# Kernel tuning notes

Measured on AMD Instinct MI355X. Metric: run time of the kernel, lower is better.

## Reference

```python
import jax, jax.numpy as jnp
import numpy as np

N_HEAD = 12

def setup_inputs() -> dict:
    key = jax.random.key(0)
    k1, k2, k3 = jax.random.split(key, 3)
    B, T, C = 4, 2048, 768
    x = jax.random.normal(k1, (B, T, C), dtype=jnp.float32)
    # c_attn params (Linear(n_embd, 3*n_embd)); stored as [in, out] for x @ W
    W_attn = jax.random.normal(k2, (C, 3 * C), dtype=jnp.float32) * (1.0 / np.sqrt(C))
    b_attn = jax.random.normal(k3, (3 * C,), dtype=jnp.float32) * 0.02
    return {"x": x, "W_attn": W_attn, "b_attn": b_attn}

def reference(x, W_attn, b_attn):
    B, T, C = x.shape
    H = N_HEAD
    Dh = C // H
    qkv = x @ W_attn + b_attn                      # [B,T,3C]
    q, k, v = jnp.split(qkv, 3, axis=-1)
    q = q.reshape(B, T, H, Dh)
    k = k.reshape(B, T, H, Dh)
    v = v.reshape(B, T, H, Dh)
    scale = 1.0 / np.sqrt(Dh)
    # scaled QK^T per head: [B,H,T,T]
    scores = jnp.einsum('bqhd,bkhd->bhqk', q * scale, k)
    causal = jnp.tril(jnp.ones((T, T), dtype=bool))  # [T,T]
    # masked-to--inf then ReLU == zero out non-causal and clamp at 0
    p = jnp.where(causal, jnp.maximum(scores, 0.0), 0.0)
    y = jnp.einsum('bhqk,bkhd->bqhd', p, v).reshape(B, T, C)
    return y
```

## Files before the change

kernel.cpp:

```cpp
#include <hip/hip_runtime.h>
#include <cstdint>
#include <cstddef>

typedef unsigned short u16;
typedef unsigned int u32;
typedef __bf16 bf16x8 __attribute__((ext_vector_type(8)));
typedef float f32x4 __attribute__((ext_vector_type(4)));

__device__ __forceinline__ u16 f2bf(float f) {
    unsigned int x = __builtin_bit_cast(unsigned int, f);
    x += 0x7FFFu + ((x >> 16) & 1u);
    return (u16)(x >> 16);
}

__device__ __forceinline__ bf16x8 ldfrag(const u16* p) {
    bf16x8 r;
    __builtin_memcpy(&r, (const u16*)__builtin_assume_aligned(p, 16), 16);
    return r;
}

__device__ __forceinline__ int4 ldg16(const u16* p) {
    int4 r;
    __builtin_memcpy(&r, (const u16*)__builtin_assume_aligned(p, 16), 16);
    return r;
}

__device__ __forceinline__ void async16(u16* lds, const u16* g) {
    __builtin_amdgcn_global_load_lds(
        (const __attribute__((address_space(1))) void*)g,
        (__attribute__((address_space(3))) void*)lds,
        16, 0, 0);
}

__global__ __launch_bounds__(256) void cvt_bf16(const float* __restrict__ in,
                                                u16* __restrict__ out, int n) {
    int i = (blockIdx.x * 256 + threadIdx.x) * 4;
    if (i >= n) return;
    float4 v = *reinterpret_cast<const float4*>(in + i);
    union { u16 e[4]; unsigned long long u; } w;
    w.e[0] = f2bf(v.x); w.e[1] = f2bf(v.y); w.e[2] = f2bf(v.z); w.e[3] = f2bf(v.w);
    *reinterpret_cast<unsigned long long*>(out + i) = w.u;
}

__global__ __launch_bounds__(256) void wt_transpose(const float* __restrict__ W,
                                                    u16* __restrict__ Wt) {
    const int R = 768, Ccols = 2304;
    __shared__ float tile[32][33];
    const int bx = blockIdx.x * 32;
    const int by = blockIdx.y * 32;
    const int tx = threadIdx.x & 31, ty = threadIdx.x >> 5;
    #pragma unroll
    for (int i = 0; i < 32; i += 8)
        tile[ty + i][tx] = W[(size_t)(by + ty + i) * Ccols + bx + tx];
    __syncthreads();
    #pragma unroll
    for (int i = 0; i < 32; i += 8)
        Wt[(size_t)(bx + ty + i) * R + by + tx] = f2bf(tile[tx][ty + i]);
}

__global__ __launch_bounds__(256) void qkv_gemm(const u16* __restrict__ A,
                                                const u16* __restrict__ Bt,
                                                const float* __restrict__ bias,
                                                u16* __restrict__ C) {
    const int N = 2304, K = 768;
    __shared__ __align__(16) u16 sA[128 * 64];
    __shared__ __align__(16) u16 sB[128 * 64];
    const int t = threadIdx.x;
    const int wave = t >> 6, lane = t & 63;
    const int quad = lane >> 4, l16 = lane & 15;
    const int wr = wave >> 1, wc = wave & 1;

    const int bid = blockIdx.x;
    const int xcd = bid & 7;
    const int idx = bid >> 3;
    const int m0 = (xcd * 8 + idx / 18) * 128;
    const int n0 = (idx % 18) * 128;

    const int srow_base = wave * 8 + (lane >> 3);
    const int schunk = lane & 7;
    const int swz = (lane >> 3) & 7;

    f32x4 acc[4][4] = {};

    for (int k0 = 0; k0 < K; k0 += 64) {
        __syncthreads();
        #pragma unroll
        for (int j = 0; j < 4; ++j) {
            const int row = j * 32 + srow_base;
            const int dch = schunk ^ swz;
            async16(sA + j * 2048 + wave * 512, A + (size_t)(m0 + row) * K + k0 + dch * 8);
            async16(sB + j * 2048 + wave * 512, Bt + (size_t)(n0 + row) * K + k0 + dch * 8);
        }
        __syncthreads();

        bf16x8 af[4][2], bfr[4][2];
        const int rsw = l16 & 7;
        #pragma unroll
        for (int i = 0; i < 4; ++i)
            #pragma unroll
            for (int h = 0; h < 2; ++h) {
                af[i][h] = ldfrag(sA + (wr * 64 + i * 16 + l16) * 64 + (((h * 4 + quad) ^ rsw) << 3));
                bfr[i][h] = ldfrag(sB + (wc * 64 + i * 16 + l16) * 64 + (((h * 4 + quad) ^ rsw) << 3));
            }
        #pragma unroll
        for (int h = 0; h < 2; ++h)
            #pragma unroll
            for (int i = 0; i < 4; ++i)
                #pragma unroll
                for (int j = 0; j < 4; ++j)
                    acc[i][j] = __builtin_amdgcn_mfma_f32_16x16x32_bf16(af[i][h], bfr[j][h], acc[i][j], 0, 0, 0);
    }

    #pragma unroll
    for (int i = 0; i < 4; ++i)
        #pragma unroll
        for (int j = 0; j < 4; ++j) {
            const int col = n0 + wc * 64 + j * 16 + l16;
            const float bc = bias[col];
            const float scale = (col < 768) ? 0.125f : 1.0f;
            #pragma unroll
            for (int r = 0; r < 4; ++r) {
                const int row = m0 + wr * 64 + i * 16 + quad * 4 + r;
                C[(size_t)row * N + col] = f2bf((acc[i][j][r] + bc) * scale);
            }
        }
}

__global__ __launch_bounds__(256, 3) void attn_kernel(const u16* __restrict__ qkv,
                                                      float* __restrict__ out) {
    const int T = 2048, C3 = 2304, Cc = 768, Dh = 64;

    const int bid = blockIdx.x;
    const int xcd = bid & 7;
    const int idx = bid >> 3;
    const int hb = xcd * 6 + (idx % 6);
    const int qa = idx / 6;
    const int qb = 31 - qa;
    const int h = hb % 12, b = hb / 12;

    const int t = threadIdx.x;
    const int wave = t >> 6, lane = t & 63;
    const int quad = lane >> 4, l16 = lane & 15;

    __shared__ __align__(16) u32 sVt[2][64 * 36];
    __shared__ __align__(16) u16 sP[128 * 72];

    const u16* qbase = qkv + (size_t)b * T * C3 + (size_t)h * Dh;
    const u16* kbase = qbase + Cc;
    const u16* vbase = qbase + 2 * Cc;

    bf16x8 qf[8][2];
    #pragma unroll
    for (int cg = 0; cg < 8; ++cg) {
        const int qrow = ((cg < 4) ? qa * 64 : (qb * 64 - 64)) + cg * 16 + l16;
        const u16* p = qbase + (size_t)qrow * C3 + quad * 8;
        qf[cg][0] = ldfrag(p);
        qf[cg][1] = ldfrag(p + 32);
    }

    f32x4 oacc[2][4] = {};

    const int tp = t & 31, dg = t >> 5;

    auto loadV = [&](int it, int4& r0, int4& r1) {
        const u16* vp = vbase + (size_t)(it * 64 + 2 * tp) * C3 + dg * 8;
        r0 = ldg16(vp);
        r1 = ldg16(vp + C3);
    };
    auto ldgK = [&](int it, bf16x8& f0, bf16x8& f1) {
        const u16* kp = kbase + (size_t)(it * 64 + wave * 16 + l16) * C3 + quad * 8;
        f0 = ldfrag(kp);
        f1 = ldfrag(kp + 32);
    };
    auto writeV = [&](int bi, const int4& r0, const int4& r1) {
        union { int4 v; u16 e[8]; } ua, ub;
        ua.v = r0; ub.v = r1;
        #pragma unroll
        for (int i = 0; i < 8; ++i)
            sVt[bi][(dg * 8 + i) * 36 + tp] = (u32)ua.e[i] | ((u32)ub.e[i] << 16);
    };

    bf16x8 kc0, kc1, kn0, kn1;
    int4 vc0, vc1, vn0, vn1;

    {
        int4 a0, a1;
        loadV(0, a0, a1);
        ldgK(0, kc0, kc1);
        writeV(0, a0, a1);
    }
    loadV(1, vc0, vc1);
    vn0 = vc0; vn1 = vc1;
    __syncthreads();

    int buf = 0;
    for (int it = 0; it <= qb; ++it) {
        const bool more  = (it < qb);
        const bool more2 = (it + 1 < qb);
        if (more2) loadV(it + 2, vn0, vn1);
        if (more)  ldgK(it + 1, kn0, kn1);

        const bool act_a = (it <= qa);

        const int cg_lo = act_a ? 0 : 4;
        __builtin_amdgcn_s_setprio(1);
        #pragma unroll
        for (int cg = 7; cg >= 0; --cg) {
            if (cg < cg_lo) break;
            f32x4 s = {};
            s = __builtin_amdgcn_mfma_f32_16x16x32_bf16(kc0, qf[cg][0], s, 0, 0, 0);
            s = __builtin_amdgcn_mfma_f32_16x16x32_bf16(kc1, qf[cg][1], s, 0, 0, 0);
            const bool diag = (cg < 4) ? (it == qa) : (it == qb);
            u32 bits[4];
            #pragma unroll
            for (int r = 0; r < 4; ++r) {
                float v = fmaxf(s[r], 0.0f);
                if (diag && (wave * 16 + quad * 4 + r > (cg & 3) * 16 + l16)) v = 0.0f;
                bits[r] = __builtin_bit_cast(u32, v);
            }
            u32 pk[2];
            pk[0] = (bits[1] & 0xFFFF0000u) | (bits[0] >> 16);
            pk[1] = (bits[3] & 0xFFFF0000u) | (bits[2] >> 16);
            __builtin_memcpy((u16*)__builtin_assume_aligned(
                                 sP + (cg * 16 + l16) * 72 + wave * 16 + quad * 4, 8),
                             pk, 8);
        }
        __builtin_amdgcn_s_setprio(0);

        asm volatile("s_waitcnt lgkmcnt(0)" ::: "memory");
        __builtin_amdgcn_s_barrier();
        asm volatile("" ::: "memory");

        const u16* sVb = (const u16*)sVt[buf];
        __builtin_amdgcn_s_setprio(1);
        #pragma unroll
        for (int kk = 0; kk < 2; ++kk) {
            bf16x8 ap1 = ldfrag(sP + (64 + wave * 16 + l16) * 72 + kk * 32 + quad * 8);
            bf16x8 ap0;
            if (act_a) ap0 = ldfrag(sP + (wave * 16 + l16) * 72 + kk * 32 + quad * 8);
            #pragma unroll
            for (int dt = 0; dt < 4; ++dt) {
                bf16x8 bv = ldfrag(sVb + (dt * 16 + l16) * 72 + kk * 32 + quad * 8);
                oacc[1][dt] = __builtin_amdgcn_mfma_f32_16x16x32_bf16(ap1, bv, oacc[1][dt], 0, 0, 0);
                if (act_a)
                    oacc[0][dt] = __builtin_amdgcn_mfma_f32_16x16x32_bf16(ap0, bv, oacc[0][dt], 0, 0, 0);
            }
        }
        __builtin_amdgcn_s_setprio(0);

        if (more) writeV(buf ^ 1, vc0, vc1);

        asm volatile("s_waitcnt lgkmcnt(0)" ::: "memory");
        __builtin_amdgcn_s_barrier();
        asm volatile("" ::: "memory");

        kc0 = kn0; kc1 = kn1;
        vc0 = vn0; vc1 = vn1;
        buf ^= 1;
    }

    #pragma unroll
    for (int g = 0; g < 2; ++g)
        #pragma unroll
        for (int dt = 0; dt < 4; ++dt)
            #pragma unroll
            for (int r = 0; r < 4; ++r) {
                const int tok = (g == 0 ? qa * 64 : qb * 64) + wave * 16 + quad * 4 + r;
                const int c = h * Dh + dt * 16 + l16;
                out[((size_t)b * T + tok) * Cc + c] = oacc[g][dt][r];
            }
}

extern "C" void kernel_launch(void* const* d_in, const int* in_sizes, int n_in,
                              void* d_out, int out_size, void* d_ws, size_t ws_size,
                              hipStream_t stream) {
    const float* x    = (const float*)d_in[0];
    const float* W    = (const float*)d_in[1];
    const float* bias = (const float*)d_in[2];
    float* out = (float*)d_out;

    char* ws = (char*)d_ws;
    const size_t xb_bytes = (size_t)8192 * 768 * 2;
    const size_t wt_bytes = (size_t)2304 * 768 * 2;
    u16* xb  = (u16*)ws;
    u16* Wt  = (u16*)(ws + xb_bytes);
    u16* qkv = (u16*)(ws + xb_bytes + wt_bytes);

    cvt_bf16<<<6144, 256, 0, stream>>>(x, xb, 8192 * 768);
    wt_transpose<<<dim3(72, 24), 256, 0, stream>>>(W, Wt);
    qkv_gemm<<<1152, 256, 0, stream>>>(xb, Wt, bias, qkv);
    attn_kernel<<<768, 256, 0, stream>>>(qkv, out);
}
```

Before: 179.2 us.

## Split paired query blocks into single-block attention CTAs and prefetch GEMM tiles

The attention kernel no longer pairs a short and a long query block per workgroup. It launches one workgroup per 64-row query block, twice as many, ordered longest-first, with half the P shared buffer and fewer registers, and raises the occupancy hint to 5. Separately, the QKV GEMM issues the next k-tile's async loads right after fragments are read into registers, so global loads overlap the MFMAs. The trade-off is that the K/V streams are loaded twice for the split blocks, and load balance now depends on the hardware scheduler instead of the explicit pairing.

```diff
diff --git a/kernel.cpp b/kernel.cpp
--- a/kernel.cpp
+++ b/kernel.cpp
@@ -79,19 +79,24 @@
     const int srow_base = wave * 8 + (lane >> 3);
     const int schunk = lane & 7;
     const int swz = (lane >> 3) & 7;
-
-    f32x4 acc[4][4] = {};
-
-    for (int k0 = 0; k0 < K; k0 += 64) {
-        __syncthreads();
+    const int dch = schunk ^ swz;
+
+    auto stage = [&](int k0) {
         #pragma unroll
         for (int j = 0; j < 4; ++j) {
             const int row = j * 32 + srow_base;
-            const int dch = schunk ^ swz;
             async16(sA + j * 2048 + wave * 512, A + (size_t)(m0 + row) * K + k0 + dch * 8);
             async16(sB + j * 2048 + wave * 512, Bt + (size_t)(n0 + row) * K + k0 + dch * 8);
         }
-        __syncthreads();
+    };
+
+    f32x4 acc[4][4] = {};
+
+    stage(0);
+    for (int k0 = 0; k0 < K; k0 += 64) {
+        asm volatile("s_waitcnt vmcnt(0)" ::: "memory");
+        __builtin_amdgcn_s_barrier();
+        asm volatile("" ::: "memory");
 
         bf16x8 af[4][2], bfr[4][2];
         const int rsw = l16 & 7;
@@ -102,6 +107,13 @@
                 af[i][h] = ldfrag(sA + (wr * 64 + i * 16 + l16) * 64 + (((h * 4 + quad) ^ rsw) << 3));
                 bfr[i][h] = ldfrag(sB + (wc * 64 + i * 16 + l16) * 64 + (((h * 4 + quad) ^ rsw) << 3));
             }
+
+        asm volatile("s_waitcnt lgkmcnt(0)" ::: "memory");
+        __builtin_amdgcn_s_barrier();
+        asm volatile("" ::: "memory");
+
+        if (k0 + 64 < K) stage(k0 + 64);
+
         #pragma unroll
         for (int h = 0; h < 2; ++h)
             #pragma unroll
@@ -126,16 +138,16 @@
         }
 }
 
-__global__ __launch_bounds__(256, 3) void attn_kernel(const u16* __restrict__ qkv,
+__global__ __launch_bounds__(256, 5) void attn_kernel(const u16* __restrict__ qkv,
                                                       float* __restrict__ out) {
     const int T = 2048, C3 = 2304, Cc = 768, Dh = 64;
 
     const int bid = blockIdx.x;
     const int xcd = bid & 7;
     const int idx = bid >> 3;
-    const int hb = xcd * 6 + (idx % 6);
-    const int qa = idx / 6;
-    const int qb = 31 - qa;
+    const int q = 31 - idx / 6;
+    const int gl = idx % 6;
+    const int hb = xcd * 6 + gl;
     const int h = hb % 12, b = hb / 12;
 
     const int t = threadIdx.x;
@@ -143,22 +155,21 @@
     const int quad = lane >> 4, l16 = lane & 15;
 
     __shared__ __align__(16) u32 sVt[2][64 * 36];
-    __shared__ __align__(16) u16 sP[128 * 72];
+    __shared__ __align__(16) u16 sP[64 * 72];
 
     const u16* qbase = qkv + (size_t)b * T * C3 + (size_t)h * Dh;
     const u16* kbase = qbase + Cc;
     const u16* vbase = qbase + 2 * Cc;
 
-    bf16x8 qf[8][2];
-    #pragma unroll
-    for (int cg = 0; cg < 8; ++cg) {
-        const int qrow = ((cg < 4) ? qa * 64 : (qb * 64 - 64)) + cg * 16 + l16;
-        const u16* p = qbase + (size_t)qrow * C3 + quad * 8;
+    bf16x8 qf[4][2];
+    #pragma unroll
+    for (int cg = 0; cg < 4; ++cg) {
+        const u16* p = qbase + (size_t)(q * 64 + cg * 16 + l16) * C3 + quad * 8;
         qf[cg][0] = ldfrag(p);
         qf[cg][1] = ldfrag(p + 32);
     }
 
-    f32x4 oacc[2][4] = {};
+    f32x4 oacc[4] = {};
 
     const int tp = t & 31, dg = t >> 5;
 
@@ -194,28 +205,24 @@
     __syncthreads();
 
     int buf = 0;
-    for (int it = 0; it <= qb; ++it) {
-        const bool more  = (it < qb);
-        const bool more2 = (it + 1 < qb);
+    for (int it = 0; it <= q; ++it) {
+        const bool more  = (it < q);
+        const bool more2 = (it + 1 < q);
         if (more2) loadV(it + 2, vn0, vn1);
         if (more)  ldgK(it + 1, kn0, kn1);
 
-        const bool act_a = (it <= qa);
-
-        const int cg_lo = act_a ? 0 : 4;
+        const bool diag = (it == q);
         __builtin_amdgcn_s_setprio(1);
         #pragma unroll
-        for (int cg = 7; cg >= 0; --cg) {
-            if (cg < cg_lo) break;
+        for (int cg = 0; cg < 4; ++cg) {
             f32x4 s = {};
             s = __builtin_amdgcn_mfma_f32_16x16x32_bf16(kc0, qf[cg][0], s, 0, 0, 0);
             s = __builtin_amdgcn_mfma_f32_16x16x32_bf16(kc1, qf[cg][1], s, 0, 0, 0);
-            const bool diag = (cg < 4) ? (it == qa) : (it == qb);
             u32 bits[4];
             #pragma unroll
             for (int r = 0; r < 4; ++r) {
                 float v = fmaxf(s[r], 0.0f);
-                if (diag && (wave * 16 + quad * 4 + r > (cg & 3) * 16 + l16)) v = 0.0f;
+                if (diag && (wave * 16 + quad * 4 + r > cg * 16 + l16)) v = 0.0f;
                 bits[r] = __builtin_bit_cast(u32, v);
             }
             u32 pk[2];
@@ -235,15 +242,11 @@
         __builtin_amdgcn_s_setprio(1);
         #pragma unroll
         for (int kk = 0; kk < 2; ++kk) {
-            bf16x8 ap1 = ldfrag(sP + (64 + wave * 16 + l16) * 72 + kk * 32 + quad * 8);
-            bf16x8 ap0;
-            if (act_a) ap0 = ldfrag(sP + (wave * 16 + l16) * 72 + kk * 32 + quad * 8);
+            bf16x8 ap = ldfrag(sP + (wave * 16 + l16) * 72 + kk * 32 + quad * 8);
             #pragma unroll
             for (int dt = 0; dt < 4; ++dt) {
                 bf16x8 bv = ldfrag(sVb + (dt * 16 + l16) * 72 + kk * 32 + quad * 8);
-                oacc[1][dt] = __builtin_amdgcn_mfma_f32_16x16x32_bf16(ap1, bv, oacc[1][dt], 0, 0, 0);
-                if (act_a)
-                    oacc[0][dt] = __builtin_amdgcn_mfma_f32_16x16x32_bf16(ap0, bv, oacc[0][dt], 0, 0, 0);
+                oacc[dt] = __builtin_amdgcn_mfma_f32_16x16x32_bf16(ap, bv, oacc[dt], 0, 0, 0);
             }
         }
         __builtin_amdgcn_s_setprio(0);
@@ -260,15 +263,13 @@
     }
 
     #pragma unroll
-    for (int g = 0; g < 2; ++g)
-        #pragma unroll
-        for (int dt = 0; dt < 4; ++dt)
-            #pragma unroll
-            for (int r = 0; r < 4; ++r) {
-                const int tok = (g == 0 ? qa * 64 : qb * 64) + wave * 16 + quad * 4 + r;
-                const int c = h * Dh + dt * 16 + l16;
-                out[((size_t)b * T + tok) * Cc + c] = oacc[g][dt][r];
-            }
+    for (int dt = 0; dt < 4; ++dt)
+        #pragma unroll
+        for (int r = 0; r < 4; ++r) {
+            const int tok = q * 64 + wave * 16 + quad * 4 + r;
+            const int c = h * Dh + dt * 16 + l16;
+            out[((size_t)b * T + tok) * Cc + c] = oacc[dt][r];
+        }
 }
 
 extern "C" void kernel_launch(void* const* d_in, const int* in_sizes, int n_in,
@@ -289,5 +290,5 @@
     cvt_bf16<<<6144, 256, 0, stream>>>(x, xb, 8192 * 768);
     wt_transpose<<<dim3(72, 24), 256, 0, stream>>>(W, Wt);
     qkv_gemm<<<1152, 256, 0, stream>>>(xb, Wt, bias, qkv);
-    attn_kernel<<<768, 256, 0, stream>>>(qkv, out);
-}
+    attn_kernel<<<1536, 256, 0, stream>>>(qkv, out);
+}
```

Result: slower. 201.2 us (+12.3%).

## Double KV tile to 128 keys per iteration and prefetch GEMM stages

Applied to the files above, without the earlier changes.

The attention kernel now processes 128 keys per loop iteration instead of 64. This halves the number of barrier-separated iterations and gives more MFMA work per sync, at the cost of larger LDS buffers, lower occupancy (launch bounds 2) and extra wasted or zero-filled MFMA work on partial tiles. The QKV GEMM is restructured to issue the next K-slice's async global-to-LDS copies after the fragments are read, so loads overlap with the MFMAs, in place of two full syncthreads per step.

```diff
diff --git a/kernel.cpp b/kernel.cpp
--- a/kernel.cpp
+++ b/kernel.cpp
@@ -79,19 +79,24 @@
     const int srow_base = wave * 8 + (lane >> 3);
     const int schunk = lane & 7;
     const int swz = (lane >> 3) & 7;
-
-    f32x4 acc[4][4] = {};
-
-    for (int k0 = 0; k0 < K; k0 += 64) {
-        __syncthreads();
+    const int dch = schunk ^ swz;
+
+    auto stage = [&](int k0) {
         #pragma unroll
         for (int j = 0; j < 4; ++j) {
             const int row = j * 32 + srow_base;
-            const int dch = schunk ^ swz;
             async16(sA + j * 2048 + wave * 512, A + (size_t)(m0 + row) * K + k0 + dch * 8);
             async16(sB + j * 2048 + wave * 512, Bt + (size_t)(n0 + row) * K + k0 + dch * 8);
         }
-        __syncthreads();
+    };
+
+    f32x4 acc[4][4] = {};
+
+    stage(0);
+    for (int k0 = 0; k0 < K; k0 += 64) {
+        asm volatile("s_waitcnt vmcnt(0)" ::: "memory");
+        __builtin_amdgcn_s_barrier();
+        asm volatile("" ::: "memory");
 
         bf16x8 af[4][2], bfr[4][2];
         const int rsw = l16 & 7;
@@ -102,6 +107,13 @@
                 af[i][h] = ldfrag(sA + (wr * 64 + i * 16 + l16) * 64 + (((h * 4 + quad) ^ rsw) << 3));
                 bfr[i][h] = ldfrag(sB + (wc * 64 + i * 16 + l16) * 64 + (((h * 4 + quad) ^ rsw) << 3));
             }
+
+        asm volatile("s_waitcnt lgkmcnt(0)" ::: "memory");
+        __builtin_amdgcn_s_barrier();
+        asm volatile("" ::: "memory");
+
+        if (k0 + 64 < K) stage(k0 + 64);
+
         #pragma unroll
         for (int h = 0; h < 2; ++h)
             #pragma unroll
@@ -126,24 +138,25 @@
         }
 }
 
-__global__ __launch_bounds__(256, 3) void attn_kernel(const u16* __restrict__ qkv,
+__global__ __launch_bounds__(256, 2) void attn_kernel(const u16* __restrict__ qkv,
                                                       float* __restrict__ out) {
     const int T = 2048, C3 = 2304, Cc = 768, Dh = 64;
 
     const int bid = blockIdx.x;
     const int xcd = bid & 7;
     const int idx = bid >> 3;
-    const int hb = xcd * 6 + (idx % 6);
     const int qa = idx / 6;
     const int qb = 31 - qa;
+    const int hb = xcd * 6 + (idx % 6);
     const int h = hb % 12, b = hb / 12;
+    const int nit = qb / 2 + 1;
 
     const int t = threadIdx.x;
     const int wave = t >> 6, lane = t & 63;
     const int quad = lane >> 4, l16 = lane & 15;
 
-    __shared__ __align__(16) u32 sVt[2][64 * 36];
-    __shared__ __align__(16) u16 sP[128 * 72];
+    __shared__ __align__(16) u32 sVt[2][64 * 68];
+    __shared__ __align__(16) u16 sP[128 * 136];
 
     const u16* qbase = qkv + (size_t)b * T * C3 + (size_t)h * Dh;
     const u16* kbase = qbase + Cc;
@@ -160,70 +173,81 @@
 
     f32x4 oacc[2][4] = {};
 
-    const int tp = t & 31, dg = t >> 5;
-
-    auto loadV = [&](int it, int4& r0, int4& r1) {
-        const u16* vp = vbase + (size_t)(it * 64 + 2 * tp) * C3 + dg * 8;
-        r0 = ldg16(vp);
-        r1 = ldg16(vp + C3);
+    auto loadV = [&](int it2, int4* r) {
+        const u16* vp = vbase + (size_t)(it2 * 128 + 2 * lane) * C3 + wave * 16;
+        r[0] = ldg16(vp);
+        r[1] = ldg16(vp + 8);
+        r[2] = ldg16(vp + C3);
+        r[3] = ldg16(vp + C3 + 8);
     };
-    auto ldgK = [&](int it, bf16x8& f0, bf16x8& f1) {
-        const u16* kp = kbase + (size_t)(it * 64 + wave * 16 + l16) * C3 + quad * 8;
-        f0 = ldfrag(kp);
-        f1 = ldfrag(kp + 32);
+    auto writeV = [&](int bi, const int4* r) {
+        union { int4 v; u16 e[8]; } u0, u1, u2, u3;
+        u0.v = r[0]; u1.v = r[1]; u2.v = r[2]; u3.v = r[3];
+        #pragma unroll
+        for (int i = 0; i < 8; ++i) {
+            sVt[bi][(wave * 16 + i) * 68 + lane]     = (u32)u0.e[i] | ((u32)u2.e[i] << 16);
+            sVt[bi][(wave * 16 + 8 + i) * 68 + lane] = (u32)u1.e[i] | ((u32)u3.e[i] << 16);
+        }
     };
-    auto writeV = [&](int bi, const int4& r0, const int4& r1) {
-        union { int4 v; u16 e[8]; } ua, ub;
-        ua.v = r0; ub.v = r1;
-        #pragma unroll
-        for (int i = 0; i < 8; ++i)
-            sVt[bi][(dg * 8 + i) * 36 + tp] = (u32)ua.e[i] | ((u32)ub.e[i] << 16);
+    auto ldgK = [&](int it2, bf16x8 k[2][2]) {
+        #pragma unroll
+        for (int s = 0; s < 2; ++s) {
+            const u16* kp = kbase + (size_t)(it2 * 128 + s * 64 + wave * 16 + l16) * C3 + quad * 8;
+            k[s][0] = ldfrag(kp);
+            k[s][1] = ldfrag(kp + 32);
+        }
     };
 
-    bf16x8 kc0, kc1, kn0, kn1;
-    int4 vc0, vc1, vn0, vn1;
+    bf16x8 kc[2][2], kn[2][2];
+    int4 vc[4], vn[4];
 
     {
-        int4 a0, a1;
-        loadV(0, a0, a1);
-        ldgK(0, kc0, kc1);
-        writeV(0, a0, a1);
+        int4 a[4];
+        loadV(0, a);
+        ldgK(0, kc);
+        writeV(0, a);
     }
-    loadV(1, vc0, vc1);
-    vn0 = vc0; vn1 = vc1;
+    loadV(1, vc);
+    #pragma unroll
+    for (int i = 0; i < 4; ++i) vn[i] = vc[i];
     __syncthreads();
 
     int buf = 0;
-    for (int it = 0; it <= qb; ++it) {
-        const bool more  = (it < qb);
-        const bool more2 = (it + 1 < qb);
-        if (more2) loadV(it + 2, vn0, vn1);
-        if (more)  ldgK(it + 1, kn0, kn1);
-
-        const bool act_a = (it <= qa);
-
-        const int cg_lo = act_a ? 0 : 4;
+    for (int it = 0; it < nit; ++it) {
+        const bool more  = (it + 1 < nit);
+        const bool more2 = (it + 2 < nit);
+        if (more2) loadV(it + 2, vn);
+        if (more)  ldgK(it + 1, kn);
+
         __builtin_amdgcn_s_setprio(1);
         #pragma unroll
-        for (int cg = 7; cg >= 0; --cg) {
-            if (cg < cg_lo) break;
-            f32x4 s = {};
-            s = __builtin_amdgcn_mfma_f32_16x16x32_bf16(kc0, qf[cg][0], s, 0, 0, 0);
-            s = __builtin_amdgcn_mfma_f32_16x16x32_bf16(kc1, qf[cg][1], s, 0, 0, 0);
-            const bool diag = (cg < 4) ? (it == qa) : (it == qb);
-            u32 bits[4];
-            #pragma unroll
-            for (int r = 0; r < 4; ++r) {
-                float v = fmaxf(s[r], 0.0f);
-                if (diag && (wave * 16 + quad * 4 + r > (cg & 3) * 16 + l16)) v = 0.0f;
-                bits[r] = __builtin_bit_cast(u32, v);
-            }
-            u32 pk[2];
-            pk[0] = (bits[1] & 0xFFFF0000u) | (bits[0] >> 16);
-            pk[1] = (bits[3] & 0xFFFF0000u) | (bits[2] >> 16);
-            __builtin_memcpy((u16*)__builtin_assume_aligned(
-                                 sP + (cg * 16 + l16) * 72 + wave * 16 + quad * 4, 8),
-                             pk, 8);
+        for (int cg = 0; cg < 8; ++cg) {
+            const int qt = (cg < 4) ? qa : qb;
+            u16* prow = sP + (((cg >> 2) * 64 + (cg & 3) * 16 + l16) * 136) + wave * 16 + quad * 4;
+            #pragma unroll
+            for (int s = 0; s < 2; ++s) {
+                const int j = 2 * it + s;
+                u16* dst = prow + s * 64;
+                if (j <= qt) {
+                    f32x4 sc = {};
+                    sc = __builtin_amdgcn_mfma_f32_16x16x32_bf16(kc[s][0], qf[cg][0], sc, 0, 0, 0);
+                    sc = __builtin_amdgcn_mfma_f32_16x16x32_bf16(kc[s][1], qf[cg][1], sc, 0, 0, 0);
+                    u32 bits[4];
+                    #pragma unroll
+                    for (int r = 0; r < 4; ++r) {
+                        float v = fmaxf(sc[r], 0.0f);
+                        if (j == qt && (wave * 16 + quad * 4 + r > (cg & 3) * 16 + l16)) v = 0.0f;
+                        bits[r] = __builtin_bit_cast(u32, v);
+                    }
+                    u32 pk[2];
+                    pk[0] = (bits[1] & 0xFFFF0000u) | (bits[0] >> 16);
+                    pk[1] = (bits[3] & 0xFFFF0000u) | (bits[2] >> 16);
+                    __builtin_memcpy((u16*)__builtin_assume_aligned(dst, 8), pk, 8);
+                } else if (j == qt + 1 || j == qt + 2) {
+                    u32 z[2] = {0, 0};
+                    __builtin_memcpy((u16*)__builtin_assume_aligned(dst, 8), z, 8);
+                }
+            }
         }
         __builtin_amdgcn_s_setprio(0);
 
@@ -231,31 +255,33 @@
         __builtin_amdgcn_s_barrier();
         asm volatile("" ::: "memory");
 
-        const u16* sVb = (const u16*)sVt[buf];
+        const u16* sVb = (const u16*)&sVt[buf][0];
         __builtin_amdgcn_s_setprio(1);
         #pragma unroll
-        for (int kk = 0; kk < 2; ++kk) {
-            bf16x8 ap1 = ldfrag(sP + (64 + wave * 16 + l16) * 72 + kk * 32 + quad * 8);
-            bf16x8 ap0;
-            if (act_a) ap0 = ldfrag(sP + (wave * 16 + l16) * 72 + kk * 32 + quad * 8);
+        for (int kk = 0; kk < 4; ++kk) {
+            bf16x8 ap0 = ldfrag(sP + (wave * 16 + l16) * 136 + kk * 32 + quad * 8);
+            bf16x8 ap1 = ldfrag(sP + (64 + wave * 16 + l16) * 136 + kk * 32 + quad * 8);
             #pragma unroll
             for (int dt = 0; dt < 4; ++dt) {
-                bf16x8 bv = ldfrag(sVb + (dt * 16 + l16) * 72 + kk * 32 + quad * 8);
+                bf16x8 bv = ldfrag(sVb + (dt * 16 + l16) * 136 + kk * 32 + quad * 8);
+                oacc[0][dt] = __builtin_amdgcn_mfma_f32_16x16x32_bf16(ap0, bv, oacc[0][dt], 0, 0, 0);
                 oacc[1][dt] = __builtin_amdgcn_mfma_f32_16x16x32_bf16(ap1, bv, oacc[1][dt], 0, 0, 0);
-                if (act_a)
-                    oacc[0][dt] = __builtin_amdgcn_mfma_f32_16x16x32_bf16(ap0, bv, oacc[0][dt], 0, 0, 0);
             }
         }
         __builtin_amdgcn_s_setprio(0);
 
-        if (more) writeV(buf ^ 1, vc0, vc1);
+        if (more) writeV(buf ^ 1, vc);
 
         asm volatile("s_waitcnt lgkmcnt(0)" ::: "memory");
         __builtin_amdgcn_s_barrier();
         asm volatile("" ::: "memory");
 
-        kc0 = kn0; kc1 = kn1;
-        vc0 = vn0; vc1 = vn1;
+        #pragma unroll
+        for (int s = 0; s < 2; ++s) {
+            kc[s][0] = kn[s][0]; kc[s][1] = kn[s][1];
+        }
+        #pragma unroll
+        for (int i = 0; i < 4; ++i) vc[i] = vn[i];
         buf ^= 1;
     }
 
```

Measured after the change: 205.4 us. 14.6% more time.
